# Performance work log

Hardware: AMD Instinct MI355X
Metric: run time of the kernel (lower is better)

The kernel has to match this reference:

```python
import jax, jax.numpy as jnp
import numpy as np

THRES = 4.0  # init kwarg Thres
EPS = 1e-10


def setup_inputs() -> dict:
    key = jax.random.key(0)
    k1, = jax.random.split(key, 1)
    xorig = jax.random.normal(k1, (4096, 16384), dtype=jnp.float32)
    gamma = jnp.ones((), dtype=jnp.float32)
    beta = jnp.zeros((), dtype=jnp.float32)
    return {"xorig": xorig, "gamma": gamma, "beta": beta}


def reference(xorig, gamma, beta):
    x = xorig.reshape(-1)
    n = x.shape[0]
    # Pass 1: global mean / unbiased variance (torch.var default unbiased=True)
    mean1 = jnp.mean(x)
    var1 = jnp.sum((x - mean1) ** 2) / (n - 1)
    normalized = (x - mean1) * jax.lax.rsqrt(var1 + EPS)
    # Outlier mask: |normalized| < Thres (strict, matching (<) * (>))
    mask = (normalized < THRES) & (normalized > -THRES)
    cnt = jnp.sum(mask).astype(x.dtype)
    # Pass 2: masked mean / unbiased variance without materializing pruned tensor
    mean2 = jnp.sum(jnp.where(mask, x, 0.0)) / cnt
    var2 = jnp.sum(jnp.where(mask, (x - mean2) ** 2, 0.0)) / (cnt - 1.0)
    # Final affine normalization over the ORIGINAL (unpruned) tensor
    return gamma * (xorig - mean2) * jax.lax.rsqrt(var2 + EPS) + beta
```

## Files before the change

### kernel.cpp

```cpp
#include <hip/hip_runtime.h>

#define THREADS 256
#define MAXBLK 2048
#define EPS 1e-10
#define THRES 4.0f

__device__ __forceinline__ double wave_sum(double v) {
#pragma unroll
  for (int off = 32; off > 0; off >>= 1)
    v += __shfl_down(v, off, 64);
  return v;
}

__device__ __forceinline__ double block_sum(double v, double* lds) {
  v = wave_sum(v);
  const int lane = threadIdx.x & 63;
  const int wid = threadIdx.x >> 6;
  __syncthreads();
  if (lane == 0) lds[wid] = v;
  __syncthreads();
  return lds[0] + lds[1] + lds[2] + lds[3];
}

__global__ void __launch_bounds__(THREADS) k_reduce1(
    const float4* __restrict__ xv, long nvec,
    const float* __restrict__ x, long n,
    double* __restrict__ pA, double* __restrict__ pB) {
  __shared__ double lds[4];
  double s = 0.0, ss = 0.0;
  const long stride = (long)gridDim.x * blockDim.x;
  const long gtid = (long)blockIdx.x * blockDim.x + threadIdx.x;
  for (long i = gtid; i < nvec; i += stride) {
    float4 v = xv[i];
    double a = v.x, b = v.y, c = v.z, d = v.w;
    s += (a + b) + (c + d);
    ss += (a * a + b * b) + (c * c + d * d);
  }
  for (long i = nvec * 4 + gtid; i < n; i += stride) {
    double a = x[i];
    s += a;
    ss += a * a;
  }
  s = block_sum(s, lds);
  ss = block_sum(ss, lds);
  if (threadIdx.x == 0) {
    pA[blockIdx.x] = s;
    pB[blockIdx.x] = ss;
  }
}

__global__ void __launch_bounds__(THREADS) k_fin1(
    const double* __restrict__ pA, const double* __restrict__ pB, int nblk,
    double n, double* __restrict__ fin) {
  __shared__ double lds[4];
  double s = 0.0, ss = 0.0;
  for (int i = threadIdx.x; i < nblk; i += blockDim.x) {
    s += pA[i];
    ss += pB[i];
  }
  s = block_sum(s, lds);
  ss = block_sum(ss, lds);
  if (threadIdx.x == 0) {
    double mean1 = s / n;
    double var1 = (ss - s * s / n) / (n - 1.0);
    fin[0] = mean1;
    fin[1] = 1.0 / sqrt(var1 + EPS);
  }
}

__global__ void __launch_bounds__(THREADS) k_reduce2(
    const float4* __restrict__ xv, long nvec,
    const float* __restrict__ x, long n,
    const double* __restrict__ fin,
    double* __restrict__ pA, double* __restrict__ pB, double* __restrict__ pC) {
  __shared__ double lds[4];
  const float m1 = (float)fin[0];
  const float r1 = (float)fin[1];
  double s = 0.0, ss = 0.0, c = 0.0;
  const long stride = (long)gridDim.x * blockDim.x;
  const long gtid = (long)blockIdx.x * blockDim.x + threadIdx.x;
  for (long i = gtid; i < nvec; i += stride) {
    float4 v = xv[i];
    float nf;
    nf = (v.x - m1) * r1;
    if (nf < THRES && nf > -THRES) { double a = v.x; s += a; ss += a * a; c += 1.0; }
    nf = (v.y - m1) * r1;
    if (nf < THRES && nf > -THRES) { double a = v.y; s += a; ss += a * a; c += 1.0; }
    nf = (v.z - m1) * r1;
    if (nf < THRES && nf > -THRES) { double a = v.z; s += a; ss += a * a; c += 1.0; }
    nf = (v.w - m1) * r1;
    if (nf < THRES && nf > -THRES) { double a = v.w; s += a; ss += a * a; c += 1.0; }
  }
  for (long i = nvec * 4 + gtid; i < n; i += stride) {
    float xf = x[i];
    float nf = (xf - m1) * r1;
    if (nf < THRES && nf > -THRES) { double a = xf; s += a; ss += a * a; c += 1.0; }
  }
  s = block_sum(s, lds);
  ss = block_sum(ss, lds);
  c = block_sum(c, lds);
  if (threadIdx.x == 0) {
    pA[blockIdx.x] = s;
    pB[blockIdx.x] = ss;
    pC[blockIdx.x] = c;
  }
}

__global__ void __launch_bounds__(THREADS) k_fin2(
    const double* __restrict__ pA, const double* __restrict__ pB,
    const double* __restrict__ pC, int nblk, double* __restrict__ fin) {
  __shared__ double lds[4];
  double s = 0.0, ss = 0.0, c = 0.0;
  for (int i = threadIdx.x; i < nblk; i += blockDim.x) {
    s += pA[i];
    ss += pB[i];
    c += pC[i];
  }
  s = block_sum(s, lds);
  ss = block_sum(ss, lds);
  c = block_sum(c, lds);
  if (threadIdx.x == 0) {
    double mean2 = s / c;
    double var2 = (ss - s * s / c) / (c - 1.0);
    fin[2] = mean2;
    fin[3] = 1.0 / sqrt(var2 + EPS);
  }
}

__global__ void __launch_bounds__(THREADS) k_apply(
    const float4* __restrict__ xv, float4* __restrict__ ov, long nvec,
    const float* __restrict__ x, float* __restrict__ o, long n,
    const double* __restrict__ fin,
    const float* __restrict__ gamma, const float* __restrict__ beta) {
  const float m2 = (float)fin[2];
  const float r2 = (float)fin[3];
  const float g = gamma[0];
  const float b = beta[0];
  const long stride = (long)gridDim.x * blockDim.x;
  const long gtid = (long)blockIdx.x * blockDim.x + threadIdx.x;
  for (long i = gtid; i < nvec; i += stride) {
    float4 v = xv[i];
    float4 t;
    t.x = g * (v.x - m2) * r2 + b;
    t.y = g * (v.y - m2) * r2 + b;
    t.z = g * (v.z - m2) * r2 + b;
    t.w = g * (v.w - m2) * r2 + b;
    ov[i] = t;
  }
  for (long i = nvec * 4 + gtid; i < n; i += stride) {
    o[i] = g * (x[i] - m2) * r2 + b;
  }
}

extern "C" void kernel_launch(void* const* d_in, const int* in_sizes, int n_in,
                              void* d_out, int out_size, void* d_ws, size_t ws_size,
                              hipStream_t stream) {
  const float* x = (const float*)d_in[0];
  const float* gamma = (const float*)d_in[1];
  const float* beta = (const float*)d_in[2];
  float* out = (float*)d_out;
  const long n = (long)in_sizes[0];
  const long nvec = n / 4;

  int nblk = MAXBLK;
  while ((size_t)(64 + 3 * (size_t)nblk * sizeof(double)) > ws_size && nblk > 64)
    nblk >>= 1;
  double* fin = (double*)d_ws;
  double* pA = (double*)((char*)d_ws + 64);
  double* pB = pA + nblk;
  double* pC = pB + nblk;

  const float4* xv = (const float4*)x;
  float4* ov = (float4*)out;

  k_reduce1<<<nblk, THREADS, 0, stream>>>(xv, nvec, x, n, pA, pB);
  k_fin1<<<1, THREADS, 0, stream>>>(pA, pB, nblk, (double)n, fin);
  k_reduce2<<<nblk, THREADS, 0, stream>>>(xv, nvec, x, n, fin, pA, pB, pC);
  k_fin2<<<1, THREADS, 0, stream>>>(pA, pB, pC, nblk, fin);
  k_apply<<<nblk, THREADS, 0, stream>>>(xv, ov, nvec, x, out, n, fin, gamma, beta);
}
```

Before: 216.0 us.

## Collect outlier candidates in first pass to skip second full-data reduction

Adds a small estimation pass over the first million elements to guess the mean and a conservative 3-sigma threshold. The first full pass then also gathers elements beyond that threshold into per-block LDS buffers. If every block stays under capacity and the threshold is provably inside the true 4-sigma bound, the masked statistics are computed as the full sums minus the sums over the outlier candidates, which skips the second full read of 256 MB. A fallback keeps the original masked pass, and the output writes become nontemporal stores. The cost is extra kernels, LDS atomics in the hot loop, and a candidate buffer in the workspace.

After: 181.7 us. -15.9%, faster.

```diff
diff --git a/kernel.cpp b/kernel.cpp
--- a/kernel.cpp
+++ b/kernel.cpp
@@ -1,14 +1,19 @@
 #include <hip/hip_runtime.h>
 
 #define THREADS 256
-#define MAXBLK 2048
+#define NBLK 2048
+#define ESTBLK 64
+#define OUTBLK 64
+#define CAP 256
+#define EST_CHUNK (1 << 20)
 #define EPS 1e-10
 #define THRES 4.0f
 
+typedef float vf4 __attribute__((ext_vector_type(4)));
+
 __device__ __forceinline__ double wave_sum(double v) {
 #pragma unroll
-  for (int off = 32; off > 0; off >>= 1)
-    v += __shfl_down(v, off, 64);
+  for (int off = 32; off > 0; off >>= 1) v += __shfl_down(v, off, 64);
   return v;
 }
 
@@ -22,6 +27,85 @@
   return lds[0] + lds[1] + lds[2] + lds[3];
 }
 
+__global__ void __launch_bounds__(THREADS) k_est(
+    const float4* __restrict__ xv, long nvec_est,
+    double* __restrict__ pEa, double* __restrict__ pEb) {
+  __shared__ double lds[4];
+  double s = 0.0, ss = 0.0;
+  const long stride = (long)gridDim.x * blockDim.x;
+  for (long i = (long)blockIdx.x * blockDim.x + threadIdx.x; i < nvec_est; i += stride) {
+    float4 v = xv[i];
+    double a = v.x, b = v.y, c = v.z, d = v.w;
+    s += (a + b) + (c + d);
+    ss += (a * a + b * b) + (c * c + d * d);
+  }
+  s = block_sum(s, lds);
+  ss = block_sum(ss, lds);
+  if (threadIdx.x == 0) { pEa[blockIdx.x] = s; pEb[blockIdx.x] = ss; }
+}
+
+__global__ void __launch_bounds__(THREADS) k_estfin(
+    const double* __restrict__ pEa, const double* __restrict__ pEb, int nblk,
+    double nest, double* __restrict__ est) {
+  __shared__ double lds[4];
+  double s = 0.0, ss = 0.0;
+  for (int i = threadIdx.x; i < nblk; i += blockDim.x) { s += pEa[i]; ss += pEb[i]; }
+  s = block_sum(s, lds);
+  ss = block_sum(ss, lds);
+  if (threadIdx.x == 0) {
+    double m = s / nest;
+    double var = (ss - s * s / nest) / (nest - 1.0);
+    double sig = var > 0.0 ? sqrt(var) : 0.0;
+    est[0] = m;
+    est[1] = 3.0 * sig;
+  }
+}
+
+__global__ void __launch_bounds__(THREADS) k_reduce1c(
+    const float4* __restrict__ xv, long nvec,
+    const float* __restrict__ x, long n,
+    const double* __restrict__ est,
+    double* __restrict__ pA, double* __restrict__ pB,
+    float* __restrict__ slices, int* __restrict__ counts) {
+  __shared__ double lds[4];
+  __shared__ int lcnt;
+  __shared__ float lcand[CAP];
+  if (threadIdx.x == 0) lcnt = 0;
+  __syncthreads();
+  const float mh = (float)est[0];
+  const float th = (float)est[1];
+  double s = 0.0, ss = 0.0;
+  const long stride = (long)gridDim.x * blockDim.x;
+  const long gtid = (long)blockIdx.x * blockDim.x + threadIdx.x;
+  for (long i = gtid; i < nvec; i += stride) {
+    float4 v = xv[i];
+    double a = v.x, b = v.y, c = v.z, d = v.w;
+    s += (a + b) + (c + d);
+    ss += (a * a + b * b) + (c * c + d * d);
+    if (fabsf(v.x - mh) > th) { int k = atomicAdd(&lcnt, 1); if (k < CAP) lcand[k] = v.x; }
+    if (fabsf(v.y - mh) > th) { int k = atomicAdd(&lcnt, 1); if (k < CAP) lcand[k] = v.y; }
+    if (fabsf(v.z - mh) > th) { int k = atomicAdd(&lcnt, 1); if (k < CAP) lcand[k] = v.z; }
+    if (fabsf(v.w - mh) > th) { int k = atomicAdd(&lcnt, 1); if (k < CAP) lcand[k] = v.w; }
+  }
+  for (long i = nvec * 4 + gtid; i < n; i += stride) {
+    float f = x[i];
+    double a = f;
+    s += a;
+    ss += a * a;
+    if (fabsf(f - mh) > th) { int k = atomicAdd(&lcnt, 1); if (k < CAP) lcand[k] = f; }
+  }
+  s = block_sum(s, lds);
+  ss = block_sum(ss, lds);
+  if (threadIdx.x == 0) {
+    pA[blockIdx.x] = s;
+    pB[blockIdx.x] = ss;
+    counts[blockIdx.x] = lcnt;
+  }
+  int c = lcnt < CAP ? lcnt : CAP;
+  for (int t = threadIdx.x; t < c; t += blockDim.x)
+    slices[(size_t)blockIdx.x * CAP + t] = lcand[t];
+}
+
 __global__ void __launch_bounds__(THREADS) k_reduce1(
     const float4* __restrict__ xv, long nvec,
     const float* __restrict__ x, long n,
@@ -43,36 +127,94 @@
   }
   s = block_sum(s, lds);
   ss = block_sum(ss, lds);
-  if (threadIdx.x == 0) {
-    pA[blockIdx.x] = s;
-    pB[blockIdx.x] = ss;
-  }
+  if (threadIdx.x == 0) { pA[blockIdx.x] = s; pB[blockIdx.x] = ss; }
 }
 
 __global__ void __launch_bounds__(THREADS) k_fin1(
     const double* __restrict__ pA, const double* __restrict__ pB, int nblk,
-    double n, double* __restrict__ fin) {
-  __shared__ double lds[4];
-  double s = 0.0, ss = 0.0;
-  for (int i = threadIdx.x; i < nblk; i += blockDim.x) {
-    s += pA[i];
-    ss += pB[i];
-  }
-  s = block_sum(s, lds);
-  ss = block_sum(ss, lds);
+    const int* __restrict__ counts, const double* __restrict__ est, int have_cand,
+    double n, double* __restrict__ fin, int* __restrict__ flag) {
+  __shared__ double lds[4];
+  __shared__ int lmx[4];
+  double s = 0.0, ss = 0.0;
+  for (int i = threadIdx.x; i < nblk; i += blockDim.x) { s += pA[i]; ss += pB[i]; }
+  s = block_sum(s, lds);
+  ss = block_sum(ss, lds);
+  int mx = 0;
+  if (have_cand) {
+    for (int i = threadIdx.x; i < nblk; i += blockDim.x) {
+      int c = counts[i];
+      mx = mx > c ? mx : c;
+    }
+  }
+#pragma unroll
+  for (int off = 32; off > 0; off >>= 1) {
+    int o = __shfl_down(mx, off, 64);
+    mx = mx > o ? mx : o;
+  }
+  __syncthreads();
+  if ((threadIdx.x & 63) == 0) lmx[threadIdx.x >> 6] = mx;
+  __syncthreads();
   if (threadIdx.x == 0) {
+    int maxcnt = lmx[0] > lmx[1] ? lmx[0] : lmx[1];
+    int m23 = lmx[2] > lmx[3] ? lmx[2] : lmx[3];
+    maxcnt = maxcnt > m23 ? maxcnt : m23;
     double mean1 = s / n;
     double var1 = (ss - s * s / n) / (n - 1.0);
+    double sig1 = var1 > 0.0 ? sqrt(var1) : 0.0;
     fin[0] = mean1;
     fin[1] = 1.0 / sqrt(var1 + EPS);
-  }
-}
-
-__global__ void __launch_bounds__(THREADS) k_reduce2(
+    fin[4] = s;
+    fin[5] = ss;
+    int ok = 0;
+    if (have_cand) {
+      double thr_hat = est[1];
+      ok = (maxcnt <= CAP) && (thr_hat > 0.0) &&
+           (thr_hat < 4.0 * sig1 * (1.0 - 1e-4) - fabs(mean1 - est[0]));
+    }
+    *flag = ok;
+  }
+}
+
+__global__ void __launch_bounds__(THREADS) k_outlier(
+    const float* __restrict__ slices, const int* __restrict__ counts, int nslices,
+    const int* __restrict__ flag, const double* __restrict__ fin,
+    double* __restrict__ pD, double* __restrict__ pE, double* __restrict__ pF) {
+  if (!*flag) return;
+  __shared__ double lds[4];
+  const float m1 = (float)fin[0];
+  const float r1 = (float)fin[1];
+  double s = 0.0, ss = 0.0, c = 0.0;
+  const long total = (long)nslices * CAP;
+  const long stride = (long)gridDim.x * blockDim.x;
+  for (long j = (long)blockIdx.x * blockDim.x + threadIdx.x; j < total; j += stride) {
+    int sl = (int)(j / CAP);
+    int t = (int)(j % CAP);
+    int cnt = counts[sl];
+    cnt = cnt < CAP ? cnt : CAP;
+    if (t < cnt) {
+      float v = slices[j];
+      float nf = (v - m1) * r1;
+      if (!(nf < THRES && nf > -THRES)) {
+        double a = v;
+        s += a;
+        ss += a * a;
+        c += 1.0;
+      }
+    }
+  }
+  s = block_sum(s, lds);
+  ss = block_sum(ss, lds);
+  c = block_sum(c, lds);
+  if (threadIdx.x == 0) { pD[blockIdx.x] = s; pE[blockIdx.x] = ss; pF[blockIdx.x] = c; }
+}
+
+__global__ void __launch_bounds__(THREADS) k_reduce2f(
     const float4* __restrict__ xv, long nvec,
     const float* __restrict__ x, long n,
-    const double* __restrict__ fin,
+    const double* __restrict__ fin, const int* __restrict__ flag,
     double* __restrict__ pA, double* __restrict__ pB, double* __restrict__ pC) {
+  if (*flag) return;
   __shared__ double lds[4];
   const float m1 = (float)fin[0];
   const float r1 = (float)fin[1];
@@ -99,26 +241,33 @@
   s = block_sum(s, lds);
   ss = block_sum(ss, lds);
   c = block_sum(c, lds);
-  if (threadIdx.x == 0) {
-    pA[blockIdx.x] = s;
-    pB[blockIdx.x] = ss;
-    pC[blockIdx.x] = c;
-  }
+  if (threadIdx.x == 0) { pA[blockIdx.x] = s; pB[blockIdx.x] = ss; pC[blockIdx.x] = c; }
 }
 
 __global__ void __launch_bounds__(THREADS) k_fin2(
     const double* __restrict__ pA, const double* __restrict__ pB,
-    const double* __restrict__ pC, int nblk, double* __restrict__ fin) {
-  __shared__ double lds[4];
-  double s = 0.0, ss = 0.0, c = 0.0;
-  for (int i = threadIdx.x; i < nblk; i += blockDim.x) {
-    s += pA[i];
-    ss += pB[i];
-    c += pC[i];
-  }
-  s = block_sum(s, lds);
-  ss = block_sum(ss, lds);
-  c = block_sum(c, lds);
+    const double* __restrict__ pC, int nblk,
+    const double* __restrict__ pD, const double* __restrict__ pE,
+    const double* __restrict__ pF, int noblk,
+    const int* __restrict__ flag, double n, double* __restrict__ fin) {
+  __shared__ double lds[4];
+  double s, ss, c;
+  if (*flag) {
+    double so = 0.0, sso = 0.0, co = 0.0;
+    for (int i = threadIdx.x; i < noblk; i += blockDim.x) { so += pD[i]; sso += pE[i]; co += pF[i]; }
+    so = block_sum(so, lds);
+    sso = block_sum(sso, lds);
+    co = block_sum(co, lds);
+    s = fin[4] - so;
+    ss = fin[5] - sso;
+    c = n - co;
+  } else {
+    double s2 = 0.0, ss2 = 0.0, c2 = 0.0;
+    for (int i = threadIdx.x; i < nblk; i += blockDim.x) { s2 += pA[i]; ss2 += pB[i]; c2 += pC[i]; }
+    s = block_sum(s2, lds);
+    ss = block_sum(ss2, lds);
+    c = block_sum(c2, lds);
+  }
   if (threadIdx.x == 0) {
     double mean2 = s / c;
     double var2 = (ss - s * s / c) / (c - 1.0);
@@ -140,15 +289,16 @@
   const long gtid = (long)blockIdx.x * blockDim.x + threadIdx.x;
   for (long i = gtid; i < nvec; i += stride) {
     float4 v = xv[i];
-    float4 t;
+    vf4 t;
     t.x = g * (v.x - m2) * r2 + b;
     t.y = g * (v.y - m2) * r2 + b;
     t.z = g * (v.z - m2) * r2 + b;
     t.w = g * (v.w - m2) * r2 + b;
-    ov[i] = t;
+    __builtin_nontemporal_store(t, (vf4*)&ov[i]);
   }
   for (long i = nvec * 4 + gtid; i < n; i += stride) {
-    o[i] = g * (x[i] - m2) * r2 + b;
+    float t = g * (x[i] - m2) * r2 + b;
+    __builtin_nontemporal_store(t, &o[i]);
   }
 }
 
@@ -161,21 +311,46 @@
   float* out = (float*)d_out;
   const long n = (long)in_sizes[0];
   const long nvec = n / 4;
-
-  int nblk = MAXBLK;
-  while ((size_t)(64 + 3 * (size_t)nblk * sizeof(double)) > ws_size && nblk > 64)
-    nblk >>= 1;
-  double* fin = (double*)d_ws;
-  double* pA = (double*)((char*)d_ws + 64);
-  double* pB = pA + nblk;
-  double* pC = pB + nblk;
-
   const float4* xv = (const float4*)x;
   float4* ov = (float4*)out;
 
-  k_reduce1<<<nblk, THREADS, 0, stream>>>(xv, nvec, x, n, pA, pB);
-  k_fin1<<<1, THREADS, 0, stream>>>(pA, pB, nblk, (double)n, fin);
-  k_reduce2<<<nblk, THREADS, 0, stream>>>(xv, nvec, x, n, fin, pA, pB, pC);
-  k_fin2<<<1, THREADS, 0, stream>>>(pA, pB, pC, nblk, fin);
-  k_apply<<<nblk, THREADS, 0, stream>>>(xv, ov, nvec, x, out, n, fin, gamma, beta);
-}
+  char* base = (char*)d_ws;
+  double* fin = (double*)base;
+  int* flag = (int*)(base + 64);
+  double* est = (double*)(base + 128);
+  double* pA = (double*)(base + 192);
+  double* pB = pA + NBLK;
+  double* pC = pB + NBLK;
+  double* pEa = pC + NBLK;
+  double* pEb = pEa + ESTBLK;
+  double* pD = pEb + ESTBLK;
+  double* pE = pD + OUTBLK;
+  double* pF = pE + OUTBLK;
+  int* counts = (int*)(pF + OUTBLK);
+  float* slices = (float*)(counts + NBLK);
+  size_t needed = (size_t)((char*)(slices + (size_t)NBLK * CAP) - base);
+
+  bool cand = (ws_size >= needed) && (n >= (long)(1 << 22));
+
+  if (cand) {
+    k_est<<<ESTBLK, THREADS, 0, stream>>>(xv, (long)(EST_CHUNK / 4), pEa, pEb);
+    k_estfin<<<1, THREADS, 0, stream>>>(pEa, pEb, ESTBLK, (double)EST_CHUNK, est);
+    k_reduce1c<<<NBLK, THREADS, 0, stream>>>(xv, nvec, x, n, est, pA, pB, slices, counts);
+    k_fin1<<<1, THREADS, 0, stream>>>(pA, pB, NBLK, counts, est, 1, (double)n, fin, flag);
+    k_outlier<<<OUTBLK, THREADS, 0, stream>>>(slices, counts, NBLK, flag, fin, pD, pE, pF);
+    k_reduce2f<<<NBLK, THREADS, 0, stream>>>(xv, nvec, x, n, fin, flag, pA, pB, pC);
+    k_fin2<<<1, THREADS, 0, stream>>>(pA, pB, pC, NBLK, pD, pE, pF, OUTBLK, flag, (double)n, fin);
+    k_apply<<<NBLK, THREADS, 0, stream>>>(xv, ov, nvec, x, out, n, fin, gamma, beta);
+  } else {
+    int nblk = NBLK;
+    while ((size_t)(192 + 3 * (size_t)nblk * sizeof(double)) > ws_size && nblk > 64) nblk >>= 1;
+    double* fA = (double*)(base + 192);
+    double* fB = fA + nblk;
+    double* fC = fB + nblk;
+    k_reduce1<<<nblk, THREADS, 0, stream>>>(xv, nvec, x, n, fA, fB);
+    k_fin1<<<1, THREADS, 0, stream>>>(fA, fB, nblk, nullptr, nullptr, 0, (double)n, fin, flag);
+    k_reduce2f<<<nblk, THREADS, 0, stream>>>(xv, nvec, x, n, fin, flag, fA, fB, fC);
+    k_fin2<<<1, THREADS, 0, stream>>>(fA, fB, fC, nblk, fA, fB, fC, nblk, flag, (double)n, fin);
+    k_apply<<<nblk, THREADS, 0, stream>>>(xv, ov, nvec, x, out, n, fin, gamma, beta);
+  }
+}
```

## Fuse passes into persistent kernel with grid sync and outlier-candidate shortcut

Applied to the files above, without the earlier changes.

Replaces five kernel launches with one persistent kernel using software grid barriers. During the first statistics pass each block estimates local mean/sigma from a sample and stashes values beyond a conservative threshold in LDS. When the global statistics prove that no non-candidate can be an outlier, the masked statistics are computed by subtracting candidate contributions instead of re-reading the tensor. This drops one full read of the input. It relies on all blocks being co-resident and keeps a full fallback pass when the bound check fails.

After: 309.9 us. +43.5%, slower.

```diff
diff --git a/kernel.cpp b/kernel.cpp
--- a/kernel.cpp
+++ b/kernel.cpp
@@ -1,14 +1,18 @@
 #include <hip/hip_runtime.h>
 
 #define THREADS 256
-#define MAXBLK 2048
+#define NBLK 512
+#define CAP 384
+#define EST_ITERS 16
 #define EPS 1e-10
 #define THRES 4.0f
+#define SMALLN (1 << 22)
+
+typedef float vf4 __attribute__((ext_vector_type(4)));
 
 __device__ __forceinline__ double wave_sum(double v) {
 #pragma unroll
-  for (int off = 32; off > 0; off >>= 1)
-    v += __shfl_down(v, off, 64);
+  for (int off = 32; off > 0; off >>= 1) v += __shfl_down(v, off, 64);
   return v;
 }
 
@@ -22,42 +26,234 @@
   return lds[0] + lds[1] + lds[2] + lds[3];
 }
 
-__global__ void __launch_bounds__(THREADS) k_reduce1(
-    const float4* __restrict__ xv, long nvec,
-    const float* __restrict__ x, long n,
-    double* __restrict__ pA, double* __restrict__ pB) {
+__device__ __forceinline__ void grid_sync(unsigned* bar, unsigned nblk) {
+  __syncthreads();
+  if (threadIdx.x == 0) {
+    __threadfence();
+    unsigned g = __hip_atomic_load(&bar[1], __ATOMIC_RELAXED, __HIP_MEMORY_SCOPE_AGENT);
+    unsigned v = __hip_atomic_fetch_add(&bar[0], 1u, __ATOMIC_ACQ_REL, __HIP_MEMORY_SCOPE_AGENT);
+    if (v == nblk - 1u) {
+      __hip_atomic_store(&bar[0], 0u, __ATOMIC_RELAXED, __HIP_MEMORY_SCOPE_AGENT);
+      __hip_atomic_store(&bar[1], g + 1u, __ATOMIC_RELEASE, __HIP_MEMORY_SCOPE_AGENT);
+    } else {
+      while (__hip_atomic_load(&bar[1], __ATOMIC_ACQUIRE, __HIP_MEMORY_SCOPE_AGENT) == g) {
+        __builtin_amdgcn_s_sleep(8);
+      }
+    }
+    __threadfence();
+  }
+  __syncthreads();
+}
+
+__global__ void k_init(unsigned* __restrict__ bar) {
+  if (threadIdx.x < 2) bar[threadIdx.x] = 0u;
+}
+
+__global__ void __launch_bounds__(THREADS, 4) k_fused(
+    const float* __restrict__ x, float* __restrict__ out, long n,
+    const float* __restrict__ gamma, const float* __restrict__ beta,
+    unsigned* __restrict__ bar,
+    double* __restrict__ pS, double* __restrict__ pSS,
+    double* __restrict__ pM, double* __restrict__ pT, int* __restrict__ pO,
+    double* __restrict__ pD, double* __restrict__ pE, double* __restrict__ pF) {
+  __shared__ double lds[4];
+  __shared__ float lcand[CAP];
+  __shared__ int lcnt;
+  const int b = blockIdx.x;
+  const unsigned nblk = gridDim.x;
+  const long nv4 = n >> 2;
+  const long vpb = (nv4 + nblk - 1) / nblk;
+  const long v0 = (long)b * vpb;
+  long v1 = v0 + vpb;
+  if (v1 > nv4) v1 = nv4;
+  const float4* xv = (const float4*)x;
+  const bool last = (b == (int)nblk - 1);
+
+  if (threadIdx.x == 0) lcnt = 0;
+  __syncthreads();
+
+  double es = 0.0, ess = 0.0;
+  long iter_end = v0 + (long)EST_ITERS * THREADS;
+  if (iter_end > v1) iter_end = v1;
+  for (long i = v0 + threadIdx.x; i < iter_end; i += THREADS) {
+    float4 v = xv[i];
+    double a = v.x, bb = v.y, c = v.z, d = v.w;
+    es += (a + bb) + (c + d);
+    ess += (a * a + bb * bb) + (c * c + d * d);
+  }
+  es = block_sum(es, lds);
+  ess = block_sum(ess, lds);
+  const long ecount = (iter_end - v0) * 4;
+  double mhat = 0.0, th = 0.0;
+  int ovf = 0;
+  if (ecount >= 4096) {
+    double ne = (double)ecount;
+    mhat = es / ne;
+    double var = (ess - es * es / ne) / (ne - 1.0);
+    double sig = var > 0.0 ? sqrt(var) : 0.0;
+    th = 3.2 * sig;
+    if (!(th > 0.0)) ovf = 1;
+  } else {
+    ovf = 1;
+  }
+  const float mhf = (float)mhat;
+  const float thf = (float)th;
+
+  double s = 0.0, ss = 0.0;
+  if (!ovf) {
+    for (long i = v0 + threadIdx.x; i < v1; i += THREADS) {
+      float4 v = xv[i];
+      double a = v.x, bb = v.y, c = v.z, d = v.w;
+      s += (a + bb) + (c + d);
+      ss += (a * a + bb * bb) + (c * c + d * d);
+      if (fabsf(v.x - mhf) > thf) { int k = atomicAdd(&lcnt, 1); if (k < CAP) lcand[k] = v.x; }
+      if (fabsf(v.y - mhf) > thf) { int k = atomicAdd(&lcnt, 1); if (k < CAP) lcand[k] = v.y; }
+      if (fabsf(v.z - mhf) > thf) { int k = atomicAdd(&lcnt, 1); if (k < CAP) lcand[k] = v.z; }
+      if (fabsf(v.w - mhf) > thf) { int k = atomicAdd(&lcnt, 1); if (k < CAP) lcand[k] = v.w; }
+    }
+    if (last) {
+      for (long i = nv4 * 4 + threadIdx.x; i < n; i += THREADS) {
+        float f = x[i];
+        double a = f;
+        s += a;
+        ss += a * a;
+        if (fabsf(f - mhf) > thf) { int k = atomicAdd(&lcnt, 1); if (k < CAP) lcand[k] = f; }
+      }
+    }
+  } else {
+    for (long i = v0 + threadIdx.x; i < v1; i += THREADS) {
+      float4 v = xv[i];
+      double a = v.x, bb = v.y, c = v.z, d = v.w;
+      s += (a + bb) + (c + d);
+      ss += (a * a + bb * bb) + (c * c + d * d);
+    }
+    if (last) {
+      for (long i = nv4 * 4 + threadIdx.x; i < n; i += THREADS) {
+        double a = x[i];
+        s += a;
+        ss += a * a;
+      }
+    }
+  }
+  s = block_sum(s, lds);
+  ss = block_sum(ss, lds);
+  if (threadIdx.x == 0) {
+    pS[b] = s;
+    pSS[b] = ss;
+    pM[b] = mhat;
+    pT[b] = th;
+    pO[b] = (ovf || lcnt > CAP) ? 1 : 0;
+  }
+
+  grid_sync(bar, nblk);
+
+  double gs = 0.0, gss = 0.0;
+  for (int i = threadIdx.x; i < (int)nblk; i += THREADS) { gs += pS[i]; gss += pSS[i]; }
+  gs = block_sum(gs, lds);
+  gss = block_sum(gss, lds);
+  const double nd = (double)n;
+  const double mean1 = gs / nd;
+  const double var1 = (gss - gs * gs / nd) / (nd - 1.0);
+  const double r1d = 1.0 / sqrt(var1 + EPS);
+  double bad = 0.0;
+  for (int i = threadIdx.x; i < (int)nblk; i += THREADS) {
+    double cond = (pT[i] + fabs(mean1 - pM[i])) * r1d;
+    if (pO[i] != 0 || !(cond < 3.999)) bad += 1.0;
+  }
+  bad = block_sum(bad, lds);
+  const bool fast = (bad == 0.0);
+  const float m1f = (float)mean1;
+  const float r1f = (float)r1d;
+
+  double os = 0.0, oss = 0.0, oc = 0.0;
+  if (fast) {
+    int cnt = lcnt < CAP ? lcnt : CAP;
+    for (int t = threadIdx.x; t < cnt; t += THREADS) {
+      float v = lcand[t];
+      float nf = (v - m1f) * r1f;
+      if (!(nf < THRES && nf > -THRES)) { double a = v; os += a; oss += a * a; oc += 1.0; }
+    }
+  } else {
+    for (long i = v0 + threadIdx.x; i < v1; i += THREADS) {
+      float4 v = xv[i];
+      float nf;
+      nf = (v.x - m1f) * r1f;
+      if (nf < THRES && nf > -THRES) { double a = v.x; os += a; oss += a * a; oc += 1.0; }
+      nf = (v.y - m1f) * r1f;
+      if (nf < THRES && nf > -THRES) { double a = v.y; os += a; oss += a * a; oc += 1.0; }
+      nf = (v.z - m1f) * r1f;
+      if (nf < THRES && nf > -THRES) { double a = v.z; os += a; oss += a * a; oc += 1.0; }
+      nf = (v.w - m1f) * r1f;
+      if (nf < THRES && nf > -THRES) { double a = v.w; os += a; oss += a * a; oc += 1.0; }
+    }
+    if (last) {
+      for (long i = nv4 * 4 + threadIdx.x; i < n; i += THREADS) {
+        float f = x[i];
+        float nf = (f - m1f) * r1f;
+        if (nf < THRES && nf > -THRES) { double a = f; os += a; oss += a * a; oc += 1.0; }
+      }
+    }
+  }
+  os = block_sum(os, lds);
+  oss = block_sum(oss, lds);
+  oc = block_sum(oc, lds);
+  if (threadIdx.x == 0) { pD[b] = os; pE[b] = oss; pF[b] = oc; }
+
+  grid_sync(bar, nblk);
+
+  double t1 = 0.0, t2 = 0.0, t3 = 0.0;
+  for (int i = threadIdx.x; i < (int)nblk; i += THREADS) { t1 += pD[i]; t2 += pE[i]; t3 += pF[i]; }
+  t1 = block_sum(t1, lds);
+  t2 = block_sum(t2, lds);
+  t3 = block_sum(t3, lds);
+  double s2, ss2, c2;
+  if (fast) { s2 = gs - t1; ss2 = gss - t2; c2 = nd - t3; }
+  else      { s2 = t1;      ss2 = t2;       c2 = t3; }
+  const double mean2 = s2 / c2;
+  const double var2 = (ss2 - s2 * s2 / c2) / (c2 - 1.0);
+  const float m2f = (float)mean2;
+  const float r2f = (float)(1.0 / sqrt(var2 + EPS));
+  const float g = gamma[0];
+  const float bb = beta[0];
+  float4* ov = (float4*)out;
+  for (long i = v0 + threadIdx.x; i < v1; i += THREADS) {
+    float4 v = xv[i];
+    vf4 t;
+    t.x = g * (v.x - m2f) * r2f + bb;
+    t.y = g * (v.y - m2f) * r2f + bb;
+    t.z = g * (v.z - m2f) * r2f + bb;
+    t.w = g * (v.w - m2f) * r2f + bb;
+    __builtin_nontemporal_store(t, (vf4*)&ov[i]);
+  }
+  if (last) {
+    for (long i = nv4 * 4 + threadIdx.x; i < n; i += THREADS) {
+      float t = g * (x[i] - m2f) * r2f + bb;
+      __builtin_nontemporal_store(t, &out[i]);
+    }
+  }
+}
+
+__global__ void __launch_bounds__(THREADS) k_r1(
+    const float* __restrict__ x, long n, double* __restrict__ pA, double* __restrict__ pB) {
   __shared__ double lds[4];
   double s = 0.0, ss = 0.0;
   const long stride = (long)gridDim.x * blockDim.x;
-  const long gtid = (long)blockIdx.x * blockDim.x + threadIdx.x;
-  for (long i = gtid; i < nvec; i += stride) {
-    float4 v = xv[i];
-    double a = v.x, b = v.y, c = v.z, d = v.w;
-    s += (a + b) + (c + d);
-    ss += (a * a + b * b) + (c * c + d * d);
-  }
-  for (long i = nvec * 4 + gtid; i < n; i += stride) {
+  for (long i = (long)blockIdx.x * blockDim.x + threadIdx.x; i < n; i += stride) {
     double a = x[i];
     s += a;
     ss += a * a;
   }
   s = block_sum(s, lds);
   ss = block_sum(ss, lds);
-  if (threadIdx.x == 0) {
-    pA[blockIdx.x] = s;
-    pB[blockIdx.x] = ss;
-  }
-}
-
-__global__ void __launch_bounds__(THREADS) k_fin1(
+  if (threadIdx.x == 0) { pA[blockIdx.x] = s; pB[blockIdx.x] = ss; }
+}
+
+__global__ void __launch_bounds__(THREADS) k_f1(
     const double* __restrict__ pA, const double* __restrict__ pB, int nblk,
     double n, double* __restrict__ fin) {
   __shared__ double lds[4];
   double s = 0.0, ss = 0.0;
-  for (int i = threadIdx.x; i < nblk; i += blockDim.x) {
-    s += pA[i];
-    ss += pB[i];
-  }
+  for (int i = threadIdx.x; i < nblk; i += blockDim.x) { s += pA[i]; ss += pB[i]; }
   s = block_sum(s, lds);
   ss = block_sum(ss, lds);
   if (threadIdx.x == 0) {
@@ -68,54 +264,31 @@
   }
 }
 
-__global__ void __launch_bounds__(THREADS) k_reduce2(
-    const float4* __restrict__ xv, long nvec,
-    const float* __restrict__ x, long n,
-    const double* __restrict__ fin,
+__global__ void __launch_bounds__(THREADS) k_r2(
+    const float* __restrict__ x, long n, const double* __restrict__ fin,
     double* __restrict__ pA, double* __restrict__ pB, double* __restrict__ pC) {
   __shared__ double lds[4];
   const float m1 = (float)fin[0];
   const float r1 = (float)fin[1];
   double s = 0.0, ss = 0.0, c = 0.0;
   const long stride = (long)gridDim.x * blockDim.x;
-  const long gtid = (long)blockIdx.x * blockDim.x + threadIdx.x;
-  for (long i = gtid; i < nvec; i += stride) {
-    float4 v = xv[i];
-    float nf;
-    nf = (v.x - m1) * r1;
-    if (nf < THRES && nf > -THRES) { double a = v.x; s += a; ss += a * a; c += 1.0; }
-    nf = (v.y - m1) * r1;
-    if (nf < THRES && nf > -THRES) { double a = v.y; s += a; ss += a * a; c += 1.0; }
-    nf = (v.z - m1) * r1;
-    if (nf < THRES && nf > -THRES) { double a = v.z; s += a; ss += a * a; c += 1.0; }
-    nf = (v.w - m1) * r1;
-    if (nf < THRES && nf > -THRES) { double a = v.w; s += a; ss += a * a; c += 1.0; }
-  }
-  for (long i = nvec * 4 + gtid; i < n; i += stride) {
-    float xf = x[i];
-    float nf = (xf - m1) * r1;
-    if (nf < THRES && nf > -THRES) { double a = xf; s += a; ss += a * a; c += 1.0; }
+  for (long i = (long)blockIdx.x * blockDim.x + threadIdx.x; i < n; i += stride) {
+    float f = x[i];
+    float nf = (f - m1) * r1;
+    if (nf < THRES && nf > -THRES) { double a = f; s += a; ss += a * a; c += 1.0; }
   }
   s = block_sum(s, lds);
   ss = block_sum(ss, lds);
   c = block_sum(c, lds);
-  if (threadIdx.x == 0) {
-    pA[blockIdx.x] = s;
-    pB[blockIdx.x] = ss;
-    pC[blockIdx.x] = c;
-  }
-}
-
-__global__ void __launch_bounds__(THREADS) k_fin2(
+  if (threadIdx.x == 0) { pA[blockIdx.x] = s; pB[blockIdx.x] = ss; pC[blockIdx.x] = c; }
+}
+
+__global__ void __launch_bounds__(THREADS) k_f2(
     const double* __restrict__ pA, const double* __restrict__ pB,
     const double* __restrict__ pC, int nblk, double* __restrict__ fin) {
   __shared__ double lds[4];
   double s = 0.0, ss = 0.0, c = 0.0;
-  for (int i = threadIdx.x; i < nblk; i += blockDim.x) {
-    s += pA[i];
-    ss += pB[i];
-    c += pC[i];
-  }
+  for (int i = threadIdx.x; i < nblk; i += blockDim.x) { s += pA[i]; ss += pB[i]; c += pC[i]; }
   s = block_sum(s, lds);
   ss = block_sum(ss, lds);
   c = block_sum(c, lds);
@@ -127,28 +300,17 @@
   }
 }
 
-__global__ void __launch_bounds__(THREADS) k_apply(
-    const float4* __restrict__ xv, float4* __restrict__ ov, long nvec,
-    const float* __restrict__ x, float* __restrict__ o, long n,
+__global__ void __launch_bounds__(THREADS) k_ap(
+    const float* __restrict__ x, float* __restrict__ out, long n,
     const double* __restrict__ fin,
     const float* __restrict__ gamma, const float* __restrict__ beta) {
   const float m2 = (float)fin[2];
   const float r2 = (float)fin[3];
   const float g = gamma[0];
-  const float b = beta[0];
+  const float bb = beta[0];
   const long stride = (long)gridDim.x * blockDim.x;
-  const long gtid = (long)blockIdx.x * blockDim.x + threadIdx.x;
-  for (long i = gtid; i < nvec; i += stride) {
-    float4 v = xv[i];
-    float4 t;
-    t.x = g * (v.x - m2) * r2 + b;
-    t.y = g * (v.y - m2) * r2 + b;
-    t.z = g * (v.z - m2) * r2 + b;
-    t.w = g * (v.w - m2) * r2 + b;
-    ov[i] = t;
-  }
-  for (long i = nvec * 4 + gtid; i < n; i += stride) {
-    o[i] = g * (x[i] - m2) * r2 + b;
+  for (long i = (long)blockIdx.x * blockDim.x + threadIdx.x; i < n; i += stride) {
+    out[i] = g * (x[i] - m2) * r2 + bb;
   }
 }
 
@@ -160,22 +322,33 @@
   const float* beta = (const float*)d_in[2];
   float* out = (float*)d_out;
   const long n = (long)in_sizes[0];
-  const long nvec = n / 4;
-
-  int nblk = MAXBLK;
-  while ((size_t)(64 + 3 * (size_t)nblk * sizeof(double)) > ws_size && nblk > 64)
-    nblk >>= 1;
-  double* fin = (double*)d_ws;
-  double* pA = (double*)((char*)d_ws + 64);
-  double* pB = pA + nblk;
-  double* pC = pB + nblk;
-
-  const float4* xv = (const float4*)x;
-  float4* ov = (float4*)out;
-
-  k_reduce1<<<nblk, THREADS, 0, stream>>>(xv, nvec, x, n, pA, pB);
-  k_fin1<<<1, THREADS, 0, stream>>>(pA, pB, nblk, (double)n, fin);
-  k_reduce2<<<nblk, THREADS, 0, stream>>>(xv, nvec, x, n, fin, pA, pB, pC);
-  k_fin2<<<1, THREADS, 0, stream>>>(pA, pB, pC, nblk, fin);
-  k_apply<<<nblk, THREADS, 0, stream>>>(xv, ov, nvec, x, out, n, fin, gamma, beta);
-}
+
+  char* base = (char*)d_ws;
+  unsigned* bar = (unsigned*)base;
+  double* pS = (double*)(base + 256);
+  double* pSS = pS + NBLK;
+  double* pM = pSS + NBLK;
+  double* pT = pM + NBLK;
+  double* pD = pT + NBLK;
+  double* pE = pD + NBLK;
+  double* pF = pE + NBLK;
+  int* pO = (int*)(pF + NBLK);
+  size_t needed = 256 + (size_t)NBLK * (7 * sizeof(double) + sizeof(int));
+
+  if (n >= SMALLN && (n >> 2) >= NBLK && ws_size >= needed) {
+    k_init<<<1, 64, 0, stream>>>(bar);
+    k_fused<<<NBLK, THREADS, 0, stream>>>(x, out, n, gamma, beta, bar,
+                                          pS, pSS, pM, pT, pO, pD, pE, pF);
+  } else {
+    int nblk = 64;
+    double* fin = (double*)(base);
+    double* fA = (double*)(base + 256);
+    double* fB = fA + nblk;
+    double* fC = fB + nblk;
+    k_r1<<<nblk, THREADS, 0, stream>>>(x, n, fA, fB);
+    k_f1<<<1, THREADS, 0, stream>>>(fA, fB, nblk, (double)n, fin);
+    k_r2<<<nblk, THREADS, 0, stream>>>(x, n, fin, fA, fB, fC);
+    k_f2<<<1, THREADS, 0, stream>>>(fA, fB, fC, nblk, fin);
+    k_ap<<<nblk, THREADS, 0, stream>>>(x, out, n, fin, gamma, beta);
+  }
+}
```
